# Kernel optimization log

Measured on AMD Instinct MI355X. Metric: run time of the kernel, lower is better.

The kernel has to match this reference:

```python
import jax, jax.numpy as jnp
import numpy as np

D_MODEL = 1024
N_HEADS = 16
D_K = D_MODEL // N_HEADS
NEG_INF = -1.0e9


def setup_inputs() -> dict:
    key = jax.random.key(0)
    ks = jax.random.split(key, 12)
    B, S = 2, 2048
    inp = {
        "q": jax.random.normal(ks[0], (B, S, D_MODEL), dtype=jnp.float32),
        "k": jax.random.normal(ks[1], (B, S, D_MODEL), dtype=jnp.float32),
        "v": jax.random.normal(ks[2], (B, S, D_MODEL), dtype=jnp.float32),
        "mask": jax.random.randint(ks[3], (B, 1, S, S), 0, 2, dtype=jnp.int32),
        "Wq": jax.random.normal(ks[4], (D_MODEL, D_MODEL), dtype=jnp.float32) / np.sqrt(D_MODEL),
        "bq": jnp.zeros((D_MODEL,), dtype=jnp.float32),
        "Wk": jax.random.normal(ks[5], (D_MODEL, D_MODEL), dtype=jnp.float32) / np.sqrt(D_MODEL),
        "bk": jnp.zeros((D_MODEL,), dtype=jnp.float32),
        "Wv": jax.random.normal(ks[6], (D_MODEL, D_MODEL), dtype=jnp.float32) / np.sqrt(D_MODEL),
        "bv": jnp.zeros((D_MODEL,), dtype=jnp.float32),
        "Wo": jax.random.normal(ks[7], (D_MODEL, D_MODEL), dtype=jnp.float32) / np.sqrt(D_MODEL),
        "bo": jnp.zeros((D_MODEL,), dtype=jnp.float32),
    }
    return inp


def _split_heads(x):
    B, S, _ = x.shape
    return x.reshape(B, S, N_HEADS, D_K).transpose(0, 2, 1, 3)  # [B,H,S,Dk]


def reference(q, k, v, mask, Wq, bq, Wk, bk, Wv, bv, Wo, bo):
    # QKV projections (nn.Linear: x @ W.T + b; here W stored as [in,out]-agnostic square)
    query = _split_heads(q @ Wq + bq)
    key_ = _split_heads(k @ Wk + bk)
    value = _split_heads(v @ Wv + bv)

    scale = 1.0 / np.sqrt(D_K).astype(np.float32)
    scores = jnp.einsum("bhqd,bhkd->bhqk", query, key_) * scale  # [B,H,S,S]
    scores = jnp.where(mask == 0, NEG_INF, scores)
    attn = jax.nn.softmax(scores, axis=-1)  # dropout is identity in eval (p=0.0)
    ctx = jnp.einsum("bhqk,bhkd->bhqd", attn, value)  # [B,H,S,Dk]

    B, H, S, Dk = ctx.shape
    ctx = ctx.transpose(0, 2, 1, 3).reshape(B, S, H * Dk)
    return ctx @ Wo + bo
```

## Files before the change

kernel.cpp:

```cpp
#include <hip/hip_runtime.h>
#include <hip/hip_bf16.h>

typedef __bf16 bf16_t;
typedef __bf16 bf16x2 __attribute__((ext_vector_type(2)));
typedef __bf16 bf16x8 __attribute__((ext_vector_type(8)));
typedef float f32x4 __attribute__((ext_vector_type(4)));
typedef float f32x16 __attribute__((ext_vector_type(16)));
typedef int intx4 __attribute__((ext_vector_type(4)));
typedef unsigned int u32;
typedef unsigned long long u64;

#define S_LEN 2048
#define DM 1024
#define NH 16
#define DK 64
#define M_ROWS 4096
#define SCALE_LOG2E 0.1803368801111204f

__device__ __forceinline__ int sw_off(int row, int col) {
  return row * 64 + ((((col >> 3) ^ row) & 7) << 3) + (col & 7);
}

__device__ __forceinline__ bf16x8 cvt8(const float4& a, const float4& b) {
  bf16x8 v;
  v[0] = (__bf16)a.x; v[1] = (__bf16)a.y; v[2] = (__bf16)a.z; v[3] = (__bf16)a.w;
  v[4] = (__bf16)b.x; v[5] = (__bf16)b.y; v[6] = (__bf16)b.z; v[7] = (__bf16)b.w;
  return v;
}

__device__ __forceinline__ void glds16(const bf16_t* g, bf16_t* l) {
  __builtin_amdgcn_global_load_lds(
      (const __attribute__((address_space(1))) void*)g,
      (__attribute__((address_space(3))) void*)l, 16, 0, 0);
}

__device__ __forceinline__ int pk2(float lo, float hi) {
  bf16x2 t;
  t[0] = (__bf16)lo;
  t[1] = (__bf16)hi;
  return __builtin_bit_cast(int, t);
}

__global__ __launch_bounds__(256) void pack_mask(
    const int* __restrict__ mask, u64* __restrict__ mb)
{
  const int wgl = blockIdx.x * 4 + (threadIdx.x >> 6);
  const int lane = threadIdx.x & 63;
  const int q = wgl & 2047;
  const int kw = (wgl >> 11) & 31;
  const int b = wgl >> 16;
  const int val = mask[((size_t)(b * S_LEN + q)) * S_LEN + kw * 64 + lane];
  const u64 bits = __ballot(val != 0);
  if (lane == 0) mb[wgl] = bits;
}

__global__ __launch_bounds__(256) void cvt_inputs(
    const float* __restrict__ q, const float* __restrict__ k,
    const float* __restrict__ v, bf16_t* __restrict__ Xb)
{
  const int z = blockIdx.y;
  const float* __restrict__ src = (z == 0) ? q : ((z == 1) ? k : v);
  const size_t idx = ((size_t)blockIdx.x * 256 + threadIdx.x) * 8;
  const float4 a = *(const float4*)&src[idx];
  const float4 b = *(const float4*)&src[idx + 4];
  *(bf16x8*)&Xb[(size_t)z * M_ROWS * DM + idx] = cvt8(a, b);
}

__global__ __launch_bounds__(256) void transw_kernel(
    const float* __restrict__ Wq, const float* __restrict__ Wk,
    const float* __restrict__ Wv, const float* __restrict__ Wo,
    bf16_t* __restrict__ Wt)
{
  const int z = blockIdx.z;
  const float* __restrict__ W = (z == 0) ? Wq : ((z == 1) ? Wk : ((z == 2) ? Wv : Wo));
  bf16_t* __restrict__ out = Wt + (size_t)z * DM * DM;
  __shared__ float tile[64][65];
  const int tx = threadIdx.x & 31, ty = threadIdx.x >> 5;
  const int k0 = blockIdx.x * 64, n0 = blockIdx.y * 64;
  #pragma unroll
  for (int j = 0; j < 8; ++j) {
    const float2 v = *(const float2*)&W[(size_t)(k0 + ty + 8 * j) * DM + n0 + tx * 2];
    tile[ty + 8 * j][tx * 2] = v.x;
    tile[ty + 8 * j][tx * 2 + 1] = v.y;
  }
  __syncthreads();
  #pragma unroll
  for (int j = 0; j < 8; ++j) {
    const int a = ty + 8 * j;
    bf16x2 p;
    p[0] = (__bf16)tile[tx * 2][a];
    p[1] = (__bf16)tile[tx * 2 + 1][a];
    *(bf16x2*)&out[(size_t)(n0 + a) * DM + k0 + tx * 2] = p;
  }
}

__device__ __forceinline__ void gemm128_body(
    const bf16_t* __restrict__ A, const bf16_t* __restrict__ Bt,
    const float* __restrict__ bias, const float scale,
    bf16_t* __restrict__ outb, float* __restrict__ outf)
{
  __shared__ __align__(16) bf16_t As[128 * 32];
  __shared__ __align__(16) bf16_t Bs[128 * 32];
  const int t = threadIdx.x, w = t >> 6, L = t & 63, quad = L >> 4, l16 = L & 15;
  const int m0 = blockIdx.x * 128, n0 = blockIdx.y * 128;
  const int mb = 64 * (w & 1), nb = 64 * (w >> 1);
  const int rowS = t >> 2, subS = (t & 3) * 8;

  f32x4 acc[4][4] = {};
  for (int k0 = 0; k0 < DM; k0 += 32) {
    __syncthreads();
    glds16(&A[(size_t)(m0 + rowS) * DM + k0 + subS],        &As[t * 8]);
    glds16(&A[(size_t)(m0 + 64 + rowS) * DM + k0 + subS],   &As[2048 + t * 8]);
    glds16(&Bt[(size_t)(n0 + rowS) * DM + k0 + subS],       &Bs[t * 8]);
    glds16(&Bt[(size_t)(n0 + 64 + rowS) * DM + k0 + subS],  &Bs[2048 + t * 8]);
    __syncthreads();
    bf16x8 af[4], bfr[4];
    #pragma unroll
    for (int mt = 0; mt < 4; ++mt)
      af[mt] = *(const bf16x8*)&As[(mb + 16 * mt + l16) * 32 + quad * 8];
    #pragma unroll
    for (int ct = 0; ct < 4; ++ct)
      bfr[ct] = *(const bf16x8*)&Bs[(nb + 16 * ct + l16) * 32 + quad * 8];
    #pragma unroll
    for (int mt = 0; mt < 4; ++mt)
      #pragma unroll
      for (int ct = 0; ct < 4; ++ct)
        acc[mt][ct] = __builtin_amdgcn_mfma_f32_16x16x32_bf16(af[mt], bfr[ct], acc[mt][ct], 0, 0, 0);
  }
  #pragma unroll
  for (int mt = 0; mt < 4; ++mt)
    #pragma unroll
    for (int ct = 0; ct < 4; ++ct)
      #pragma unroll
      for (int r = 0; r < 4; ++r) {
        const int row = m0 + mb + 16 * mt + quad * 4 + r;
        const int n = n0 + nb + 16 * ct + l16;
        const float val = (acc[mt][ct][r] + bias[n]) * scale;
        if (outb) outb[(size_t)row * DM + n] = (__bf16)val;
        else      outf[(size_t)row * DM + n] = val;
      }
}

__global__ __launch_bounds__(256) void gemm_qkv(
    const bf16_t* __restrict__ Xb, const bf16_t* __restrict__ Wt,
    const float* __restrict__ bq, const float* __restrict__ bk,
    const float* __restrict__ bv, bf16_t* __restrict__ QKVb)
{
  const int z = blockIdx.z;
  gemm128_body(Xb + (size_t)z * M_ROWS * DM, Wt + (size_t)z * DM * DM,
               (z == 0) ? bq : ((z == 1) ? bk : bv),
               (z == 0) ? SCALE_LOG2E : 1.0f,
               QKVb + (size_t)z * M_ROWS * DM, nullptr);
}

__global__ __launch_bounds__(256) void gemm_out(
    const bf16_t* __restrict__ ctx, const bf16_t* __restrict__ Wto,
    const float* __restrict__ bo, float* __restrict__ out)
{
  gemm128_body(ctx, Wto, bo, 1.0f, nullptr, out);
}

__global__ __launch_bounds__(256) void transpV(
    const bf16_t* __restrict__ Vb, bf16_t* __restrict__ Vtw)
{
  __shared__ bf16_t Tr[64 * 72];
  const int t = threadIdx.x;
  const int key0 = blockIdx.x * 64;
  const int bh = blockIdx.y, b = bh >> 4, h = bh & 15;
  const int r = t >> 2, c = (t & 3) * 16;
  const bf16_t* src = &Vb[(size_t)(b * S_LEN + key0 + r) * DM + h * DK + c];
  const bf16x8 v0 = *(const bf16x8*)src;
  const bf16x8 v1 = *(const bf16x8*)(src + 8);
  #pragma unroll
  for (int j = 0; j < 8; ++j) {
    Tr[r * 72 + c + j] = v0[j];
    Tr[r * 72 + c + 8 + j] = v1[j];
  }
  __syncthreads();
  const int dv = t >> 2, kc = (t & 3) * 16;
  bf16_t ov[16];
  #pragma unroll
  for (int j = 0; j < 16; ++j) ov[j] = Tr[(kc + j) * 72 + dv];
  bf16_t* dst = &Vtw[((size_t)bh * DK + dv) * S_LEN + key0 + kc];
  *(bf16x8*)dst = *(bf16x8*)&ov[0];
  *(bf16x8*)(dst + 8) = *(bf16x8*)&ov[8];
}

__global__ __launch_bounds__(512, 2) void attn_kernel(
    const bf16_t* __restrict__ Qb, const bf16_t* __restrict__ Kb,
    const bf16_t* __restrict__ Vtw, const u64* __restrict__ mb,
    bf16_t* __restrict__ ctx)
{
  __shared__ __align__(16) bf16_t KVs[2][4][64 * 64];

  const int t = threadIdx.x, w = t >> 6, L = t & 63;
  const int l31 = L & 31, h5 = L >> 5;
  const int g = blockIdx.x;
  const int xcd = g & 7, slot = g >> 3;
  const int bh = xcd * 4 + (slot >> 3), qt = slot & 7;
  const int q0 = qt * 256;
  const int b = bh >> 4, h = bh & 15;

  const int qr = q0 + 32 * w + l31;
  bf16x8 qf[4];
  {
    const bf16_t* qsrc = &Qb[(size_t)(b * S_LEN + qr) * DM + h * DK + 8 * h5];
    #pragma unroll
    for (int ks = 0; ks < 4; ++ks) qf[ks] = *(const bf16x8*)(qsrc + 16 * ks);
  }

  const int rk = t >> 3;
  const int ck = (t & 7) ^ (rk & 7);
  const bf16_t* pK = &Kb[(size_t)(b * S_LEN + rk) * DM + h * DK + ck * 8];
  const bf16_t* pV = &Vtw[((size_t)bh * DK + rk) * S_LEN + ck * 8];
  const u64* pm = &mb[(size_t)b * 32 * S_LEN + qr];

  f32x16 O[2] = {};
  float l_lane = 0.f;

  auto compute = [&](const bf16_t* __restrict__ Kc, const bf16_t* __restrict__ Vc,
                     u64 mcur) {
    f32x16 s0 = {}, s1 = {};
    #pragma unroll
    for (int ks = 0; ks < 4; ++ks) {
      const bf16x8 kf0 = *(const bf16x8*)&Kc[sw_off(l31, ks * 16 + 8 * h5)];
      const bf16x8 kf1 = *(const bf16x8*)&Kc[sw_off(32 + l31, ks * 16 + 8 * h5)];
      s0 = __builtin_amdgcn_mfma_f32_32x32x16_bf16(kf0, qf[ks], s0, 0, 0, 0);
      s1 = __builtin_amdgcn_mfma_f32_32x32x16_bf16(kf1, qf[ks], s1, 0, 0, 0);
    }
    #pragma unroll
    for (int nt = 0; nt < 2; ++nt) {
      const u32 mm = ((u32)(mcur >> (nt ? 32 : 0))) >> (4 * h5);
      const f32x16 sacc = nt ? s1 : s0;
      float p[16];
      #pragma unroll
      for (int r = 0; r < 16; ++r) {
        const int cb = (r & 3) + 8 * (r >> 2);
        const u32 mr = (u32)(((int)(mm << (31 - cb))) >> 31);
        const float e = __builtin_exp2f(sacc[r]);
        const float pv = __builtin_bit_cast(float, __builtin_bit_cast(u32, e) & mr);
        l_lane += pv;
        p[r] = pv;
      }
      #pragma unroll
      for (int ss = 0; ss < 2; ++ss) {
        const int x0 = pk2(p[8 * ss + 0], p[8 * ss + 1]);
        const int x1 = pk2(p[8 * ss + 2], p[8 * ss + 3]);
        const int y0 = pk2(p[8 * ss + 4], p[8 * ss + 5]);
        const int y1 = pk2(p[8 * ss + 6], p[8 * ss + 7]);
        const auto r0 = __builtin_amdgcn_permlane32_swap(x0, y0, false, false);
        const auto r1 = __builtin_amdgcn_permlane32_swap(x1, y1, false, false);
        intx4 wv;
        wv[0] = r0[0]; wv[1] = r1[0]; wv[2] = r0[1]; wv[3] = r1[1];
        const bf16x8 pf = __builtin_bit_cast(bf16x8, wv);
        const int s4 = 2 * nt + ss;
        const bf16x8 vf0 = *(const bf16x8*)&Vc[sw_off(l31, s4 * 16 + 8 * h5)];
        const bf16x8 vf1 = *(const bf16x8*)&Vc[sw_off(32 + l31, s4 * 16 + 8 * h5)];
        O[0] = __builtin_amdgcn_mfma_f32_32x32x16_bf16(vf0, pf, O[0], 0, 0, 0);
        O[1] = __builtin_amdgcn_mfma_f32_32x32x16_bf16(vf1, pf, O[1], 0, 0, 0);
      }
    }
  };

  bf16x8 k0r = *(const bf16x8*)pK;
  bf16x8 k1r = *(const bf16x8*)(pK + (size_t)64 * DM);
  bf16x8 v0r = *(const bf16x8*)pV;
  bf16x8 v1r = *(const bf16x8*)(pV + 64);
  u64 m0 = pm[0], m1 = pm[S_LEN];
  pK += (size_t)128 * DM; pV += 128; pm += 2 * S_LEN;
  *(bf16x8*)&KVs[0][0][t * 8] = k0r;
  *(bf16x8*)&KVs[0][1][t * 8] = k1r;
  *(bf16x8*)&KVs[0][2][t * 8] = v0r;
  *(bf16x8*)&KVs[0][3][t * 8] = v1r;
  __syncthreads();

  for (int kt = 0; kt < S_LEN / 128; ++kt) {
    const int cur = kt & 1;
    u64 n0 = 0, n1 = 0;
    if (kt + 1 < S_LEN / 128) {
      k0r = *(const bf16x8*)pK;
      k1r = *(const bf16x8*)(pK + (size_t)64 * DM);
      v0r = *(const bf16x8*)pV;
      v1r = *(const bf16x8*)(pV + 64);
      n0 = pm[0]; n1 = pm[S_LEN];
      pK += (size_t)128 * DM; pV += 128; pm += 2 * S_LEN;
    }
    compute(&KVs[cur][0][0], &KVs[cur][2][0], m0);
    compute(&KVs[cur][1][0], &KVs[cur][3][0], m1);
    if (kt + 1 < S_LEN / 128) {
      *(bf16x8*)&KVs[cur ^ 1][0][t * 8] = k0r;
      *(bf16x8*)&KVs[cur ^ 1][1][t * 8] = k1r;
      *(bf16x8*)&KVs[cur ^ 1][2][t * 8] = v0r;
      *(bf16x8*)&KVs[cur ^ 1][3][t * 8] = v1r;
      m0 = n0; m1 = n1;
    }
    __syncthreads();
  }

  const float lsum = l_lane + __shfl_xor(l_lane, 32);
  const float inv = 1.f / lsum;
  bf16_t* sc = &KVs[0][0][0] + (size_t)w * 2048;
  #pragma unroll
  for (int ot = 0; ot < 2; ++ot)
    #pragma unroll
    for (int r = 0; r < 16; ++r) {
      const int dv = 32 * ot + (r & 3) + 8 * (r >> 2) + 4 * h5;
      sc[sw_off(l31, dv)] = (__bf16)(O[ot][r] * inv);
    }
  const int erow = L >> 1, ecol = (L & 1) * 32;
  bf16_t* dst = &ctx[(size_t)(b * S_LEN + q0 + 32 * w + erow) * DM + h * DK + ecol];
  #pragma unroll
  for (int c8 = 0; c8 < 4; ++c8)
    *(bf16x8*)(dst + 8 * c8) = *(const bf16x8*)&sc[sw_off(erow, ecol + 8 * c8)];
}

extern "C" void kernel_launch(void* const* d_in, const int* in_sizes, int n_in,
                              void* d_out, int out_size, void* d_ws, size_t ws_size,
                              hipStream_t stream) {
  const float* q  = (const float*)d_in[0];
  const float* k  = (const float*)d_in[1];
  const float* v  = (const float*)d_in[2];
  const int* mask = (const int*)d_in[3];
  const float* Wq = (const float*)d_in[4];
  const float* bq = (const float*)d_in[5];
  const float* Wk = (const float*)d_in[6];
  const float* bk = (const float*)d_in[7];
  const float* Wv = (const float*)d_in[8];
  const float* bv = (const float*)d_in[9];
  const float* Wo = (const float*)d_in[10];
  const float* bo = (const float*)d_in[11];
  float* out = (float*)d_out;

  const size_t SLICE = (size_t)M_ROWS * DM;
  bf16_t* Xb   = (bf16_t*)d_ws;
  bf16_t* QKVb = Xb + 3 * SLICE;
  bf16_t* Wt   = QKVb + 3 * SLICE;
  u64* mbw     = (u64*)(Wt + (size_t)4 * DM * DM);
  bf16_t* ctx  = Xb;
  bf16_t* Vtw  = Xb + SLICE;

  pack_mask<<<dim3(32768), dim3(256), 0, stream>>>(mask, mbw);
  cvt_inputs<<<dim3(2048, 3), dim3(256), 0, stream>>>(q, k, v, Xb);
  transw_kernel<<<dim3(16, 16, 4), dim3(256), 0, stream>>>(Wq, Wk, Wv, Wo, Wt);
  gemm_qkv<<<dim3(32, 8, 3), dim3(256), 0, stream>>>(Xb, Wt, bq, bk, bv, QKVb);
  transpV<<<dim3(32, 32), dim3(256), 0, stream>>>(QKVb + 2 * SLICE, Vtw);
  attn_kernel<<<dim3(256), dim3(512), 0, stream>>>(QKVb, QKVb + SLICE, Vtw, mbw, ctx);
  gemm_out<<<dim3(32, 8), dim3(256), 0, stream>>>(ctx, Wt + (size_t)3 * DM * DM, bo, out);
}
```

Measured before the change: 287.4 us.

## Merge preprocessing kernels into one launch and deepen GEMM K-tile with swizzled LDS

Folds the three preprocessing kernels (mask packing, input fp32-to-bf16 conversion, weight transpose) into a single launch that branches on block index, removing two kernel launches and the gaps between them. Separately, the shared GEMM body now stages 64-wide K tiles instead of 32, using an XOR-swizzled LDS layout, which halves the number of barrier pairs per K loop and is meant to cut LDS bank conflicts. The larger tiles double LDS use per block, which may reduce occupancy. The combined prep kernel also reserves 64x65 floats of shared memory in every block, including those that never use it.

```diff
diff --git a/kernel.cpp b/kernel.cpp
--- a/kernel.cpp
+++ b/kernel.cpp
@@ -41,56 +41,55 @@
   return __builtin_bit_cast(int, t);
 }
 
-__global__ __launch_bounds__(256) void pack_mask(
-    const int* __restrict__ mask, u64* __restrict__ mb)
-{
-  const int wgl = blockIdx.x * 4 + (threadIdx.x >> 6);
-  const int lane = threadIdx.x & 63;
-  const int q = wgl & 2047;
-  const int kw = (wgl >> 11) & 31;
-  const int b = wgl >> 16;
-  const int val = mask[((size_t)(b * S_LEN + q)) * S_LEN + kw * 64 + lane];
-  const u64 bits = __ballot(val != 0);
-  if (lane == 0) mb[wgl] = bits;
-}
-
-__global__ __launch_bounds__(256) void cvt_inputs(
+__global__ __launch_bounds__(256) void prep(
     const float* __restrict__ q, const float* __restrict__ k,
-    const float* __restrict__ v, bf16_t* __restrict__ Xb)
-{
-  const int z = blockIdx.y;
-  const float* __restrict__ src = (z == 0) ? q : ((z == 1) ? k : v);
-  const size_t idx = ((size_t)blockIdx.x * 256 + threadIdx.x) * 8;
-  const float4 a = *(const float4*)&src[idx];
-  const float4 b = *(const float4*)&src[idx + 4];
-  *(bf16x8*)&Xb[(size_t)z * M_ROWS * DM + idx] = cvt8(a, b);
-}
-
-__global__ __launch_bounds__(256) void transw_kernel(
+    const float* __restrict__ v, bf16_t* __restrict__ Xb,
     const float* __restrict__ Wq, const float* __restrict__ Wk,
     const float* __restrict__ Wv, const float* __restrict__ Wo,
-    bf16_t* __restrict__ Wt)
-{
-  const int z = blockIdx.z;
-  const float* __restrict__ W = (z == 0) ? Wq : ((z == 1) ? Wk : ((z == 2) ? Wv : Wo));
-  bf16_t* __restrict__ out = Wt + (size_t)z * DM * DM;
+    bf16_t* __restrict__ Wt,
+    const int* __restrict__ mask, u64* __restrict__ mb)
+{
   __shared__ float tile[64][65];
-  const int tx = threadIdx.x & 31, ty = threadIdx.x >> 5;
-  const int k0 = blockIdx.x * 64, n0 = blockIdx.y * 64;
-  #pragma unroll
-  for (int j = 0; j < 8; ++j) {
-    const float2 v = *(const float2*)&W[(size_t)(k0 + ty + 8 * j) * DM + n0 + tx * 2];
-    tile[ty + 8 * j][tx * 2] = v.x;
-    tile[ty + 8 * j][tx * 2 + 1] = v.y;
-  }
-  __syncthreads();
-  #pragma unroll
-  for (int j = 0; j < 8; ++j) {
-    const int a = ty + 8 * j;
-    bf16x2 p;
-    p[0] = (__bf16)tile[tx * 2][a];
-    p[1] = (__bf16)tile[tx * 2 + 1][a];
-    *(bf16x2*)&out[(size_t)(n0 + a) * DM + k0 + tx * 2] = p;
+  const int blk = blockIdx.x;
+  if (blk < 6144) {
+    const int z = blk >> 11;
+    const int bx = blk & 2047;
+    const float* __restrict__ src = (z == 0) ? q : ((z == 1) ? k : v);
+    const size_t idx = ((size_t)bx * 256 + threadIdx.x) * 8;
+    const float4 a = *(const float4*)&src[idx];
+    const float4 b = *(const float4*)&src[idx + 4];
+    *(bf16x8*)&Xb[(size_t)z * M_ROWS * DM + idx] = cvt8(a, b);
+  } else if (blk < 7168) {
+    const int idx = blk - 6144;
+    const int z = idx >> 8, by = (idx >> 4) & 15, bx = idx & 15;
+    const float* __restrict__ W = (z == 0) ? Wq : ((z == 1) ? Wk : ((z == 2) ? Wv : Wo));
+    bf16_t* __restrict__ out = Wt + (size_t)z * DM * DM;
+    const int tx = threadIdx.x & 31, ty = threadIdx.x >> 5;
+    const int k0 = bx * 64, n0 = by * 64;
+    #pragma unroll
+    for (int j = 0; j < 8; ++j) {
+      const float2 vv = *(const float2*)&W[(size_t)(k0 + ty + 8 * j) * DM + n0 + tx * 2];
+      tile[ty + 8 * j][tx * 2] = vv.x;
+      tile[ty + 8 * j][tx * 2 + 1] = vv.y;
+    }
+    __syncthreads();
+    #pragma unroll
+    for (int j = 0; j < 8; ++j) {
+      const int a = ty + 8 * j;
+      bf16x2 p;
+      p[0] = (__bf16)tile[tx * 2][a];
+      p[1] = (__bf16)tile[tx * 2 + 1][a];
+      *(bf16x2*)&out[(size_t)(n0 + a) * DM + k0 + tx * 2] = p;
+    }
+  } else {
+    const int wgl = (blk - 7168) * 4 + (threadIdx.x >> 6);
+    const int lane = threadIdx.x & 63;
+    const int qq = wgl & 2047;
+    const int kw = (wgl >> 11) & 31;
+    const int b = wgl >> 16;
+    const int val = mask[((size_t)(b * S_LEN + qq)) * S_LEN + kw * 64 + lane];
+    const u64 bits = __ballot(val != 0);
+    if (lane == 0) mb[wgl] = bits;
   }
 }
 
@@ -99,33 +98,38 @@
     const float* __restrict__ bias, const float scale,
     bf16_t* __restrict__ outb, float* __restrict__ outf)
 {
-  __shared__ __align__(16) bf16_t As[128 * 32];
-  __shared__ __align__(16) bf16_t Bs[128 * 32];
+  __shared__ __align__(16) bf16_t As[128 * 64];
+  __shared__ __align__(16) bf16_t Bs[128 * 64];
   const int t = threadIdx.x, w = t >> 6, L = t & 63, quad = L >> 4, l16 = L & 15;
   const int m0 = blockIdx.x * 128, n0 = blockIdx.y * 128;
   const int mb = 64 * (w & 1), nb = 64 * (w >> 1);
-  const int rowS = t >> 2, subS = (t & 3) * 8;
+  const int rowS = t >> 3;
+  const int ck = (((t & 7) ^ (rowS & 7)) << 3);
 
   f32x4 acc[4][4] = {};
-  for (int k0 = 0; k0 < DM; k0 += 32) {
+  for (int k0 = 0; k0 < DM; k0 += 64) {
     __syncthreads();
-    glds16(&A[(size_t)(m0 + rowS) * DM + k0 + subS],        &As[t * 8]);
-    glds16(&A[(size_t)(m0 + 64 + rowS) * DM + k0 + subS],   &As[2048 + t * 8]);
-    glds16(&Bt[(size_t)(n0 + rowS) * DM + k0 + subS],       &Bs[t * 8]);
-    glds16(&Bt[(size_t)(n0 + 64 + rowS) * DM + k0 + subS],  &Bs[2048 + t * 8]);
+    #pragma unroll
+    for (int j = 0; j < 4; ++j) {
+      glds16(&A[(size_t)(m0 + 32 * j + rowS) * DM + k0 + ck],  &As[j * 2048 + t * 8]);
+      glds16(&Bt[(size_t)(n0 + 32 * j + rowS) * DM + k0 + ck], &Bs[j * 2048 + t * 8]);
+    }
     __syncthreads();
-    bf16x8 af[4], bfr[4];
-    #pragma unroll
-    for (int mt = 0; mt < 4; ++mt)
-      af[mt] = *(const bf16x8*)&As[(mb + 16 * mt + l16) * 32 + quad * 8];
-    #pragma unroll
-    for (int ct = 0; ct < 4; ++ct)
-      bfr[ct] = *(const bf16x8*)&Bs[(nb + 16 * ct + l16) * 32 + quad * 8];
-    #pragma unroll
-    for (int mt = 0; mt < 4; ++mt)
+    #pragma unroll
+    for (int kk = 0; kk < 2; ++kk) {
+      bf16x8 af[4], bfr[4];
+      #pragma unroll
+      for (int mt = 0; mt < 4; ++mt)
+        af[mt] = *(const bf16x8*)&As[sw_off(mb + 16 * mt + l16, kk * 32 + quad * 8)];
       #pragma unroll
       for (int ct = 0; ct < 4; ++ct)
-        acc[mt][ct] = __builtin_amdgcn_mfma_f32_16x16x32_bf16(af[mt], bfr[ct], acc[mt][ct], 0, 0, 0);
+        bfr[ct] = *(const bf16x8*)&Bs[sw_off(nb + 16 * ct + l16, kk * 32 + quad * 8)];
+      #pragma unroll
+      for (int mt = 0; mt < 4; ++mt)
+        #pragma unroll
+        for (int ct = 0; ct < 4; ++ct)
+          acc[mt][ct] = __builtin_amdgcn_mfma_f32_16x16x32_bf16(af[mt], bfr[ct], acc[mt][ct], 0, 0, 0);
+    }
   }
   #pragma unroll
   for (int mt = 0; mt < 4; ++mt)
@@ -339,9 +343,8 @@
   bf16_t* ctx  = Xb;
   bf16_t* Vtw  = Xb + SLICE;
 
-  pack_mask<<<dim3(32768), dim3(256), 0, stream>>>(mask, mbw);
-  cvt_inputs<<<dim3(2048, 3), dim3(256), 0, stream>>>(q, k, v, Xb);
-  transw_kernel<<<dim3(16, 16, 4), dim3(256), 0, stream>>>(Wq, Wk, Wv, Wo, Wt);
+  prep<<<dim3(39936), dim3(256), 0, stream>>>(q, k, v, Xb, Wq, Wk, Wv, Wo, Wt,
+                                              mask, mbw);
   gemm_qkv<<<dim3(32, 8, 3), dim3(256), 0, stream>>>(Xb, Wt, bq, bk, bv, QKVb);
   transpV<<<dim3(32, 32), dim3(256), 0, stream>>>(QKVb + 2 * SLICE, Vtw);
   attn_kernel<<<dim3(256), dim3(512), 0, stream>>>(QKVb, QKVb + SLICE, Vtw, mbw, ctx);
```

Result: no change. 288.9 us (+0.5%).
